# Kernel optimization log

Hardware: AMD Instinct MI355X
Metric: run time of the kernel (lower is better)

Reference implementation:

```python
import jax, jax.numpy as jnp
import numpy as np


def setup_inputs() -> dict:
    key = jax.random.key(0)
    k1, k2, k3, k4, k5 = jax.random.split(key, 5)
    B, S, K, N, G = 4, 2048, 4096, 4096, 64  # G = group_size -> num_groups = K // G = 64
    x = jax.random.normal(k1, (B, S, K), dtype=jnp.float32)
    # int2 codes stored one-per-int8 slot (low 2 bits valid); use int32 container
    weight_q = jax.random.randint(k2, (N, K), 0, 4, dtype=jnp.int32)
    scale = jax.random.uniform(k3, (N, K // G), dtype=jnp.float32) * 0.05 + 0.01
    zp = jax.random.uniform(k4, (N, K // G), dtype=jnp.float32) * 3.0
    bias = jax.random.normal(k5, (N,), dtype=jnp.float32)
    return {"x": x, "weight_q": weight_q, "scale": scale, "zp": zp, "bias": bias}


def _dequant(weight_q, scale, zp):
    # weight_q: [N, K] int codes in [0,4); scale/zp: [N, num_groups]
    N, K = weight_q.shape
    num_groups = scale.shape[1]
    gs = K // num_groups  # group_size
    q = weight_q.astype(jnp.float32).reshape(N, num_groups, gs)
    w = (q - zp[:, :, None]) * scale[:, :, None]
    return w.reshape(N, K)


def reference(x, weight_q, scale, zp, bias):
    # asymm_qw2_gemm: out = x @ dequant(W)^T + bias
    w = _dequant(weight_q, scale, zp)            # [N, K]
    out = jnp.einsum('bsk,nk->bsn', x, w)        # [B, S, N]
    return out + bias
```

## Files before the change

kernel.cpp:

```cpp
#include <hip/hip_runtime.h>
#include <stdint.h>


typedef __attribute__((ext_vector_type(4))) float  f32x4;
typedef __attribute__((ext_vector_type(4))) int    i32x4;
typedef __attribute__((ext_vector_type(8))) __bf16 bf16x8;
typedef __attribute__((ext_vector_type(8))) unsigned short u16x8;

__device__ __forceinline__ unsigned short f2bf(float f) {
  unsigned u = __builtin_bit_cast(unsigned, f);
  u += 0x7fffu + ((u >> 16) & 1u);
  return (unsigned short)(u >> 16);
}

__device__ __forceinline__ void async16(const void* g, void* l) {
  __builtin_amdgcn_global_load_lds(
      (const __attribute__((address_space(1))) unsigned int*)g,
      (__attribute__((address_space(3))) unsigned int*)l, 16, 0, 0);
}

__global__ __launch_bounds__(256) void cvt_x_kernel(
    const float* __restrict__ x, unsigned short* __restrict__ xb, int total8) {
  int i = blockIdx.x * 256 + threadIdx.x;
  if (i >= total8) return;
  const f32x4* p = (const f32x4*)x + (size_t)i * 2;
  f32x4 a = p[0], b = p[1];
  u16x8 o;
  o[0] = f2bf(a[0]); o[1] = f2bf(a[1]); o[2] = f2bf(a[2]); o[3] = f2bf(a[3]);
  o[4] = f2bf(b[0]); o[5] = f2bf(b[1]); o[6] = f2bf(b[2]); o[7] = f2bf(b[3]);
  *(u16x8*)(xb + (size_t)i * 8) = o;
}

__global__ __launch_bounds__(256) void dequant_w_kernel(
    const int* __restrict__ q, const float* __restrict__ scale,
    const float* __restrict__ zp, unsigned short* __restrict__ wb,
    int N, int K, int G) {
  int kchunks = K / 8;
  int i = blockIdx.x * 256 + threadIdx.x;
  if (i >= N * kchunks) return;
  int n = i / kchunks, kc = i % kchunks;
  int k0 = kc * 8;
  int ng = K / G;
  int g = k0 / G;
  float s = scale[(size_t)n * ng + g];
  float b = -zp[(size_t)n * ng + g] * s;
  const i32x4* qp = (const i32x4*)(q + (size_t)n * K + k0);
  i32x4 q0 = qp[0], q1 = qp[1];
  u16x8 o;
  o[0] = f2bf((float)q0[0] * s + b); o[1] = f2bf((float)q0[1] * s + b);
  o[2] = f2bf((float)q0[2] * s + b); o[3] = f2bf((float)q0[3] * s + b);
  o[4] = f2bf((float)q1[0] * s + b); o[5] = f2bf((float)q1[1] * s + b);
  o[6] = f2bf((float)q1[2] * s + b); o[7] = f2bf((float)q1[3] * s + b);
  *(u16x8*)(wb + (size_t)i * 8) = o;
}

#define BM 128
#define BN 128
#define BK 32

__global__ __launch_bounds__(256, 2) void gemm_bt_kernel(
    const unsigned short* __restrict__ A,
    const unsigned short* __restrict__ B,
    const float* __restrict__ bias,
    float* __restrict__ C, int M, int N, int K) {
  __shared__ unsigned short As[BM * BK];
  __shared__ unsigned short Bs[BN * BK];

  const int tid  = threadIdx.x;
  const int lane = tid & 63;
  const int wave = tid >> 6;
  const int wm = wave >> 1, wn = wave & 1;
  const int q = lane >> 4, r = lane & 15;
  const int m0 = blockIdx.y * BM;
  const int n0 = blockIdx.x * BN;

  const int srow = tid >> 2, schunk = tid & 3;
  const unsigned short* aG0 = A + (size_t)(m0 + srow) * K      + schunk * 8;
  const unsigned short* aG1 = A + (size_t)(m0 + 64 + srow) * K + schunk * 8;
  const unsigned short* bG0 = B + (size_t)(n0 + srow) * K      + schunk * 8;
  const unsigned short* bG1 = B + (size_t)(n0 + 64 + srow) * K + schunk * 8;
  unsigned short* aL0 = &As[tid * 8];
  unsigned short* aL1 = &As[2048 + tid * 8];
  unsigned short* bL0 = &Bs[tid * 8];
  unsigned short* bL1 = &Bs[2048 + tid * 8];

  f32x4 acc[4][4] = {};

#pragma unroll 1
  for (int kk = 0; kk < K; kk += BK) {
    async16(aG0 + kk, aL0);
    async16(aG1 + kk, aL1);
    async16(bG0 + kk, bL0);
    async16(bG1 + kk, bL1);
    __syncthreads();

    bf16x8 af[4], bf[4];
#pragma unroll
    for (int i = 0; i < 4; ++i) {
      af[i] = *(const bf16x8*)&As[(wm * 64 + i * 16 + r) * BK + q * 8];
      bf[i] = *(const bf16x8*)&Bs[(wn * 64 + i * 16 + r) * BK + q * 8];
    }
#pragma unroll
    for (int i = 0; i < 4; ++i)
#pragma unroll
      for (int j = 0; j < 4; ++j)
        acc[i][j] = __builtin_amdgcn_mfma_f32_16x16x32_bf16(af[i], bf[j], acc[i][j], 0, 0, 0);
    __syncthreads();
  }

  float bv[4];
#pragma unroll
  for (int j = 0; j < 4; ++j) bv[j] = bias[n0 + wn * 64 + j * 16 + r];
#pragma unroll
  for (int i = 0; i < 4; ++i) {
    int mbase = m0 + wm * 64 + i * 16 + q * 4;
#pragma unroll
    for (int e = 0; e < 4; ++e) {
      float* crow = C + (size_t)(mbase + e) * N + n0 + wn * 64 + r;
#pragma unroll
      for (int j = 0; j < 4; ++j)
        crow[j * 16] = acc[i][j][e] + bv[j];
    }
  }
}

__global__ __launch_bounds__(256) void naive_kernel(
    const float* __restrict__ x, const int* __restrict__ wq,
    const float* __restrict__ scale, const float* __restrict__ zp,
    const float* __restrict__ bias, float* __restrict__ out,
    int M, int N, int K, int G) {
  int idx = blockIdx.x * 256 + threadIdx.x;
  if (idx >= M * N) return;
  int m = idx / N, n = idx % N;
  const float* xr = x + (size_t)m * K;
  const int* wr = wq + (size_t)n * K;
  int ng = K / G;
  float acc = 0.f;
  for (int g = 0; g < ng; ++g) {
    float s = scale[(size_t)n * ng + g];
    float b = -zp[(size_t)n * ng + g] * s;
    for (int k = 0; k < G; ++k)
      acc += xr[g * G + k] * ((float)wr[g * G + k] * s + b);
  }
  out[idx] = acc + bias[n];
}

extern "C" void kernel_launch(void* const* d_in, const int* in_sizes, int n_in,
                              void* d_out, int out_size, void* d_ws, size_t ws_size,
                              hipStream_t stream) {
  const float* x     = (const float*)d_in[0];
  const int*   wq    = (const int*)d_in[1];
  const float* scale = (const float*)d_in[2];
  const float* zp    = (const float*)d_in[3];
  const float* bias  = (const float*)d_in[4];
  float* out = (float*)d_out;

  const int N  = in_sizes[4];
  const int K  = in_sizes[1] / N;
  const int ng = in_sizes[2] / N;
  const int G  = K / ng;
  const int M  = in_sizes[0] / K;

  size_t xb_bytes = (size_t)M * K * 2;
  size_t wb_bytes = (size_t)N * K * 2;
  if (ws_size < xb_bytes + wb_bytes) {
    int total = M * N;
    naive_kernel<<<dim3((total + 255) / 256), dim3(256), 0, stream>>>(
        x, wq, scale, zp, bias, out, M, N, K, G);
    return;
  }

  unsigned short* xb = (unsigned short*)d_ws;
  unsigned short* wb = (unsigned short*)((char*)d_ws + xb_bytes);

  int xt = M * K / 8;
  cvt_x_kernel<<<dim3((xt + 255) / 256), dim3(256), 0, stream>>>(x, xb, xt);
  int wt = N * K / 8;
  dequant_w_kernel<<<dim3((wt + 255) / 256), dim3(256), 0, stream>>>(wq, scale, zp, wb, N, K, G);

  dim3 grid(N / BN, M / BM);
  gemm_bt_kernel<<<grid, dim3(256), 0, stream>>>(xb, wb, bias, out, M, N, K);
}
```

Measured before the change: 567.4 us.

## Swizzle GEMM LDS tiles and merge conversion kernels into one prep launch

Applies an XOR swizzle to the 16-byte chunk index when loading A/B tiles into LDS and when reading MFMA fragments, to reduce LDS bank conflicts on the fragment reads. Also merges the x-to-bf16 conversion and the weight dequantization into a single launch that splits by block index, and narrows each thread to 4 elements so accesses are more coalesced. This removes one kernel launch at the cost of more threads and slightly more index arithmetic.

```diff
diff --git a/kernel.cpp b/kernel.cpp
--- a/kernel.cpp
+++ b/kernel.cpp
@@ -5,7 +5,7 @@
 typedef __attribute__((ext_vector_type(4))) float  f32x4;
 typedef __attribute__((ext_vector_type(4))) int    i32x4;
 typedef __attribute__((ext_vector_type(8))) __bf16 bf16x8;
-typedef __attribute__((ext_vector_type(8))) unsigned short u16x8;
+typedef __attribute__((ext_vector_type(4))) unsigned short u16x4;
 
 __device__ __forceinline__ unsigned short f2bf(float f) {
   unsigned u = __builtin_bit_cast(unsigned, f);
@@ -19,39 +19,34 @@
       (__attribute__((address_space(3))) unsigned int*)l, 16, 0, 0);
 }
 
-__global__ __launch_bounds__(256) void cvt_x_kernel(
-    const float* __restrict__ x, unsigned short* __restrict__ xb, int total8) {
-  int i = blockIdx.x * 256 + threadIdx.x;
-  if (i >= total8) return;
-  const f32x4* p = (const f32x4*)x + (size_t)i * 2;
-  f32x4 a = p[0], b = p[1];
-  u16x8 o;
-  o[0] = f2bf(a[0]); o[1] = f2bf(a[1]); o[2] = f2bf(a[2]); o[3] = f2bf(a[3]);
-  o[4] = f2bf(b[0]); o[5] = f2bf(b[1]); o[6] = f2bf(b[2]); o[7] = f2bf(b[3]);
-  *(u16x8*)(xb + (size_t)i * 8) = o;
-}
-
-__global__ __launch_bounds__(256) void dequant_w_kernel(
-    const int* __restrict__ q, const float* __restrict__ scale,
+__global__ __launch_bounds__(256) void prep_kernel(
+    const float* __restrict__ x, unsigned short* __restrict__ xb, int xchunks,
+    const int* __restrict__ wq, const float* __restrict__ scale,
     const float* __restrict__ zp, unsigned short* __restrict__ wb,
-    int N, int K, int G) {
-  int kchunks = K / 8;
-  int i = blockIdx.x * 256 + threadIdx.x;
-  if (i >= N * kchunks) return;
-  int n = i / kchunks, kc = i % kchunks;
-  int k0 = kc * 8;
-  int ng = K / G;
-  int g = k0 / G;
-  float s = scale[(size_t)n * ng + g];
-  float b = -zp[(size_t)n * ng + g] * s;
-  const i32x4* qp = (const i32x4*)(q + (size_t)n * K + k0);
-  i32x4 q0 = qp[0], q1 = qp[1];
-  u16x8 o;
-  o[0] = f2bf((float)q0[0] * s + b); o[1] = f2bf((float)q0[1] * s + b);
-  o[2] = f2bf((float)q0[2] * s + b); o[3] = f2bf((float)q0[3] * s + b);
-  o[4] = f2bf((float)q1[0] * s + b); o[5] = f2bf((float)q1[1] * s + b);
-  o[6] = f2bf((float)q1[2] * s + b); o[7] = f2bf((float)q1[3] * s + b);
-  *(u16x8*)(wb + (size_t)i * 8) = o;
+    int wchunks, int K, int G) {
+  int xblocks = (xchunks + 255) >> 8;
+  if ((int)blockIdx.x < xblocks) {
+    int i = blockIdx.x * 256 + threadIdx.x;
+    if (i >= xchunks) return;
+    f32x4 a = ((const f32x4*)x)[i];
+    u16x4 o;
+    o[0] = f2bf(a[0]); o[1] = f2bf(a[1]); o[2] = f2bf(a[2]); o[3] = f2bf(a[3]);
+    *(u16x4*)(xb + (size_t)i * 4) = o;
+  } else {
+    int i = (blockIdx.x - xblocks) * 256 + threadIdx.x;
+    if (i >= wchunks) return;
+    int k4 = i * 4;
+    int n = k4 / K, kk = k4 % K;
+    int ng = K / G;
+    int g = kk / G;
+    float s = scale[(size_t)n * ng + g];
+    float b = -zp[(size_t)n * ng + g] * s;
+    i32x4 qv = ((const i32x4*)wq)[i];
+    u16x4 o;
+    o[0] = f2bf((float)qv[0] * s + b); o[1] = f2bf((float)qv[1] * s + b);
+    o[2] = f2bf((float)qv[2] * s + b); o[3] = f2bf((float)qv[3] * s + b);
+    *(u16x4*)(wb + (size_t)i * 4) = o;
+  }
 }
 
 #define BM 128
@@ -75,14 +70,17 @@
   const int n0 = blockIdx.x * BN;
 
   const int srow = tid >> 2, schunk = tid & 3;
-  const unsigned short* aG0 = A + (size_t)(m0 + srow) * K      + schunk * 8;
-  const unsigned short* aG1 = A + (size_t)(m0 + 64 + srow) * K + schunk * 8;
-  const unsigned short* bG0 = B + (size_t)(n0 + srow) * K      + schunk * 8;
-  const unsigned short* bG1 = B + (size_t)(n0 + 64 + srow) * K + schunk * 8;
+  const int gchunk = schunk ^ ((srow >> 1) & 3);
+  const unsigned short* aG0 = A + (size_t)(m0 + srow) * K      + gchunk * 8;
+  const unsigned short* aG1 = A + (size_t)(m0 + 64 + srow) * K + gchunk * 8;
+  const unsigned short* bG0 = B + (size_t)(n0 + srow) * K      + gchunk * 8;
+  const unsigned short* bG1 = B + (size_t)(n0 + 64 + srow) * K + gchunk * 8;
   unsigned short* aL0 = &As[tid * 8];
   unsigned short* aL1 = &As[2048 + tid * 8];
   unsigned short* bL0 = &Bs[tid * 8];
   unsigned short* bL1 = &Bs[2048 + tid * 8];
+
+  const int qc = (q ^ ((r >> 1) & 3)) * 8;
 
   f32x4 acc[4][4] = {};
 
@@ -97,8 +95,8 @@
     bf16x8 af[4], bf[4];
 #pragma unroll
     for (int i = 0; i < 4; ++i) {
-      af[i] = *(const bf16x8*)&As[(wm * 64 + i * 16 + r) * BK + q * 8];
-      bf[i] = *(const bf16x8*)&Bs[(wn * 64 + i * 16 + r) * BK + q * 8];
+      af[i] = *(const bf16x8*)&As[(wm * 64 + i * 16 + r) * BK + qc];
+      bf[i] = *(const bf16x8*)&Bs[(wn * 64 + i * 16 + r) * BK + qc];
     }
 #pragma unroll
     for (int i = 0; i < 4; ++i)
@@ -173,10 +171,12 @@
   unsigned short* xb = (unsigned short*)d_ws;
   unsigned short* wb = (unsigned short*)((char*)d_ws + xb_bytes);
 
-  int xt = M * K / 8;
-  cvt_x_kernel<<<dim3((xt + 255) / 256), dim3(256), 0, stream>>>(x, xb, xt);
-  int wt = N * K / 8;
-  dequant_w_kernel<<<dim3((wt + 255) / 256), dim3(256), 0, stream>>>(wq, scale, zp, wb, N, K, G);
+  int xchunks = M * K / 4;
+  int wchunks = N * K / 4;
+  int xblocks = (xchunks + 255) / 256;
+  int wblocks = (wchunks + 255) / 256;
+  prep_kernel<<<dim3(xblocks + wblocks), dim3(256), 0, stream>>>(
+      x, xb, xchunks, wq, scale, zp, wb, wchunks, K, G);
 
   dim3 grid(N / BN, M / BM);
   gemm_bt_kernel<<<grid, dim3(256), 0, stream>>>(xb, wb, bias, out, M, N, K);
```

Measured after the change: 561.4 us. About the same (-1.0%).
